# Kernel tuning notes

Measured on AMD Instinct MI355X. Metric: run time of the kernel, lower is better.

Reference implementation:

```python
import jax, jax.numpy as jnp
import numpy as np

B, T, S = 1, 8, 1024
HID, H = 1152, 16
D = HID // H  # 72
EPS = 1e-6


def rmsnorm(t, gamma):
    # t: [b,t,s,h,d], gamma: [h,d] per-head learnable scale (QKNorm)
    var = jnp.mean(jnp.square(t), axis=-1, keepdims=True)
    return t * jax.lax.rsqrt(var + EPS) * gamma


def setup_inputs() -> dict:
    key = jax.random.key(0)
    ks = jax.random.split(key, 8)
    sc = lambda fan_in: 1.0 / np.sqrt(fan_in)
    x = jax.random.normal(ks[0], (B, T, S, HID), dtype=jnp.float32)
    Wq = jax.random.normal(ks[1], (HID, HID), dtype=jnp.float32) * sc(HID)
    bq = jnp.zeros((HID,), dtype=jnp.float32)
    Wkv = jax.random.normal(ks[2], (HID, 2 * HID), dtype=jnp.float32) * sc(HID)
    bkv = jnp.zeros((2 * HID,), dtype=jnp.float32)
    q_gamma = jnp.ones((H, D), dtype=jnp.float32)
    k_gamma = jnp.ones((H, D), dtype=jnp.float32)
    Wo = jax.random.normal(ks[3], (HID, HID), dtype=jnp.float32) * sc(HID)
    return {"x": x, "Wq": Wq, "bq": bq, "Wkv": Wkv, "bkv": bkv,
            "q_gamma": q_gamma, "k_gamma": k_gamma, "Wo": Wo}


def reference(x, Wq, bq, Wkv, bkv, q_gamma, k_gamma, Wo):
    b, t, s, _ = x.shape
    q = (x @ Wq + bq).reshape(b, t, s, H, D)
    kv = x @ Wkv + bkv
    k, v = jnp.split(kv, 2, axis=-1)
    k = k.reshape(b, t, s, H, D)
    v = v.reshape(b, t, s, H, D)
    q = rmsnorm(q, q_gamma)
    k = rmsnorm(k, k_gamma)
    # NOTE: original applies no 1/sqrt(d) scaling (QKNorm replaces it)
    attn_weight = jnp.einsum('btqhd,btkhd->bthqk', q, k)
    attn = jax.nn.softmax(attn_weight, axis=-1)
    out = jnp.einsum('bthqk,btkhd->btqhd', attn, v).reshape(b, t, s, HID)
    return out @ Wo
```

## Files before the change

### kernel.cpp

```cpp
#include <hip/hip_runtime.h>


typedef __attribute__((ext_vector_type(4))) short s16x4;
typedef __attribute__((ext_vector_type(8))) short s16x8;
typedef __attribute__((ext_vector_type(4))) float f32x4;
typedef __attribute__((ext_vector_type(16))) float f32x16;

__device__ __forceinline__ unsigned short f2b(float x) {
  unsigned u = __float_as_uint(x);
  u += 0x7FFFu + ((u >> 16) & 1u);
  return (unsigned short)(u >> 16);
}
__device__ __forceinline__ float b2f(unsigned short u) {
  return __uint_as_float(((unsigned)u) << 16);
}
__device__ __forceinline__ void gld16(const void* g, void* l) {
  __builtin_amdgcn_global_load_lds(
      (const __attribute__((address_space(1))) void*)g,
      (__attribute__((address_space(3))) void*)l, 16, 0, 0);
}

__global__ __launch_bounds__(256) void cvt_bf16_kernel(const float* __restrict__ in,
                                                       unsigned short* __restrict__ out,
                                                       int n16) {
  int i = blockIdx.x * 256 + threadIdx.x;
  if (i >= n16) return;
  const float4* p = (const float4*)(in + (size_t)i * 16);
  float4 a = p[0], b = p[1], c = p[2], d = p[3];
  s16x8 r0, r1;
  r0[0] = (short)f2b(a.x); r0[1] = (short)f2b(a.y); r0[2] = (short)f2b(a.z); r0[3] = (short)f2b(a.w);
  r0[4] = (short)f2b(c.x); r0[5] = (short)f2b(c.y); r0[6] = (short)f2b(c.z); r0[7] = (short)f2b(c.w);
  r1[0] = (short)f2b(b.x); r1[1] = (short)f2b(b.y); r1[2] = (short)f2b(b.z); r1[3] = (short)f2b(b.w);
  r1[4] = (short)f2b(d.x); r1[5] = (short)f2b(d.y); r1[6] = (short)f2b(d.z); r1[7] = (short)f2b(d.w);
  *(s16x8*)(out + (size_t)i * 16) = r0;
  *(s16x8*)(out + (size_t)i * 16 + 8) = r1;
}

__global__ __launch_bounds__(256) void transpose_cvt_kernel(const float* __restrict__ W,
                                                            unsigned short* __restrict__ WT,
                                                            int K, int N) {
  __shared__ float tile[32][33];
  int n0 = blockIdx.x * 32, k0 = blockIdx.y * 32;
  int tx = threadIdx.x, ty = threadIdx.y;
#pragma unroll
  for (int i = 0; i < 4; i++)
    tile[ty + i * 8][tx] = W[(size_t)(k0 + ty + i * 8) * N + n0 + tx];
  __syncthreads();
  int stx = (tx & 19) | ((tx & 4) << 1) | ((tx & 8) >> 1);
#pragma unroll
  for (int i = 0; i < 4; i++)
    WT[(size_t)(n0 + ty + i * 8) * K + k0 + stx] = f2b(tile[tx][ty + i * 8]);
}

__global__ __launch_bounds__(256) void gemm_qkv_kernel(const unsigned short* __restrict__ A,
                                                       const unsigned short* __restrict__ BT,
                                                       const float* __restrict__ biasq,
                                                       const float* __restrict__ biaskv,
                                                       unsigned short* __restrict__ qn,
                                                       unsigned short* __restrict__ kn,
                                                       unsigned short* __restrict__ vt) {
  constexpr int K = 1152;
  constexpr int NT = K / 32;
  __shared__ __align__(16) unsigned short As[3 * 8192];
  __shared__ __align__(16) unsigned short Bs[3 * 4096];
  int tid = threadIdx.x;
  int lane = tid & 63, wave = tid >> 6;
  int wr = (wave >> 1) * 128, wc = (wave & 1) * 64;
  int l31 = lane & 31, lh = lane >> 5;
  int bid = blockIdx.x;
  int xcd = bid & 7;
  int w = bid >> 3;
  int st = w / 12, inner = w - st * 12;
  int ibx = inner % 3, iby = inner / 3;
  int bx = st * 3 + ibx;
  int by = xcd * 4 + iby;
  int brow = by * 256, bcol = bx * 128;
  const unsigned short* AsrcP[4];
  const unsigned short* BsrcP[2];
  int dstA[4], dstB[2];
#pragma unroll
  for (int i = 0; i < 4; i++) {
    int c = tid + 256 * i;
    int row = c >> 2, j = c & 3;
    AsrcP[i] = A + (size_t)(brow + row) * K + (j ^ ((row >> 1) & 3)) * 8;
    dstA[i] = (wave * 64 + 256 * i) * 8;
  }
#pragma unroll
  for (int i = 0; i < 2; i++) {
    int c = tid + 256 * i;
    int row = c >> 2, j = c & 3;
    BsrcP[i] = BT + (size_t)(bcol + row) * K + (j ^ ((row >> 1) & 3)) * 8;
    dstB[i] = (wave * 64 + 256 * i) * 8;
  }
#define STAGE(KT, BUF)                                           \
  {                                                              \
    int kb = (KT) * 32;                                          \
    gld16(AsrcP[0] + kb, &As[(BUF) * 8192 + dstA[0]]);           \
    gld16(AsrcP[1] + kb, &As[(BUF) * 8192 + dstA[1]]);           \
    gld16(AsrcP[2] + kb, &As[(BUF) * 8192 + dstA[2]]);           \
    gld16(AsrcP[3] + kb, &As[(BUF) * 8192 + dstA[3]]);           \
    gld16(BsrcP[0] + kb, &Bs[(BUF) * 4096 + dstB[0]]);           \
    gld16(BsrcP[1] + kb, &Bs[(BUF) * 4096 + dstB[1]]);           \
  }
  int fr = (l31 >> 1) & 3;
  int slotk[2] = {(lh ^ fr) * 8, ((2 + lh) ^ fr) * 8};
  STAGE(0, 0);
  STAGE(1, 1);
  f32x16 acc[4][2] = {};
  int cur = 0;
  for (int kt = 0; kt < NT; kt++) {
    if (kt < NT - 1)
      asm volatile("s_waitcnt vmcnt(6)\n\ts_barrier" ::: "memory");
    else
      asm volatile("s_waitcnt vmcnt(0)\n\ts_barrier" ::: "memory");
    if (kt + 2 < NT) {
      int nb = (cur == 0) ? 2 : cur - 1;
      STAGE(kt + 2, nb);
    }
    int ab = cur * 8192, bb = cur * 4096;
#pragma unroll
    for (int kk = 0; kk < 2; kk++) {
      int so = slotk[kk];
      s16x8 af[4], bf[2];
#pragma unroll
      for (int m = 0; m < 4; m++)
        af[m] = *(const s16x8*)&As[ab + (wr + m * 32 + l31) * 32 + so];
#pragma unroll
      for (int n = 0; n < 2; n++)
        bf[n] = *(const s16x8*)&Bs[bb + (wc + n * 32 + l31) * 32 + so];
      __builtin_amdgcn_s_setprio(1);
#pragma unroll
      for (int m = 0; m < 4; m++)
#pragma unroll
        for (int n = 0; n < 2; n++)
          acc[m][n] = __builtin_amdgcn_mfma_f32_32x32x16_bf16(af[m], bf[n], acc[m][n], 0, 0, 0);
      __builtin_amdgcn_s_setprio(0);
    }
    cur = (cur == 2) ? 0 : cur + 1;
  }
#undef STAGE
#pragma unroll
  for (int m = 0; m < 4; m++) {
#pragma unroll
    for (int n = 0; n < 2; n++) {
#pragma unroll
      for (int reg = 0; reg < 16; reg++) {
        int grow = brow + wr + m * 32 + (reg & 3) + 8 * (reg >> 2) + 4 * lh;
        int gcol = bcol + wc + n * 32 + l31;
        float v = acc[m][n][reg];
        v += (gcol < 1152) ? biasq[gcol] : biaskv[gcol - 1152];
        int t = grow >> 10, s = grow & 1023;
        if (gcol < 2304) {
          int c = (gcol < 1152) ? gcol : gcol - 1152;
          int h = c / 72, d = c - h * 72;
          unsigned short* dst = (gcol < 1152) ? qn : kn;
          dst[((size_t)((t * 16 + h) * 1024 + s)) * 96 + d] = f2b(v);
        } else {
          int c = gcol - 2304;
          int h = c / 72, d = c - h * 72;
          vt[((size_t)((t * 16 + h) * 80 + d)) * 1024 + s] = f2b(v);
        }
      }
    }
  }
}

__global__ __launch_bounds__(256) void gemm_out_kernel(const unsigned short* __restrict__ A,
                                                       const unsigned short* __restrict__ BT,
                                                       int N, int gx,
                                                       float* __restrict__ outF) {
  constexpr int K = 1152;
  constexpr int NT = K / 32;
  __shared__ __align__(16) unsigned short As[3 * 4096];
  __shared__ __align__(16) unsigned short Bs[3 * 4096];
  int tid = threadIdx.x;
  int lane = tid & 63, wave = tid >> 6;
  int wr = (wave >> 1) * 64, wc = (wave & 1) * 64;
  int l31 = lane & 31, lh = lane >> 5;
  int bid = blockIdx.x;
  int xcd = bid & 7;
  int w = bid >> 3;
  int st = w / 24, inner = w - st * 24;
  int ibx = inner % 3, iby = inner / 3;
  int bx = st * 3 + ibx;
  int by = xcd * 8 + iby;
  int brow = by * 128, bcol = bx * 128;
  const unsigned short* AsrcP[2];
  const unsigned short* BsrcP[2];
  int dst0[2];
#pragma unroll
  for (int i = 0; i < 2; i++) {
    int c = tid + 256 * i;
    int row = c >> 2, j = c & 3;
    int ch = j ^ ((row >> 1) & 3);
    AsrcP[i] = A + (size_t)(brow + row) * K + ch * 8;
    BsrcP[i] = BT + (size_t)(bcol + row) * K + ch * 8;
    dst0[i] = (wave * 64 + 256 * i) * 8;
  }
#define STAGE(KT, BUF)                                          \
  {                                                             \
    int kb = (KT) * 32;                                         \
    gld16(AsrcP[0] + kb, &As[(BUF) * 4096 + dst0[0]]);          \
    gld16(BsrcP[0] + kb, &Bs[(BUF) * 4096 + dst0[0]]);          \
    gld16(AsrcP[1] + kb, &As[(BUF) * 4096 + dst0[1]]);          \
    gld16(BsrcP[1] + kb, &Bs[(BUF) * 4096 + dst0[1]]);          \
  }
  int fr = (l31 >> 1) & 3;
  int slotk[2] = {(lh ^ fr) * 8, ((2 + lh) ^ fr) * 8};
  STAGE(0, 0);
  STAGE(1, 1);
  f32x16 acc[2][2] = {};
  int cur = 0;
  for (int kt = 0; kt < NT; kt++) {
    if (kt < NT - 1)
      asm volatile("s_waitcnt vmcnt(4)\n\ts_barrier" ::: "memory");
    else
      asm volatile("s_waitcnt vmcnt(0)\n\ts_barrier" ::: "memory");
    if (kt + 2 < NT) {
      int nb = (cur == 0) ? 2 : cur - 1;
      STAGE(kt + 2, nb);
    }
    int ab = cur * 4096;
#pragma unroll
    for (int kk = 0; kk < 2; kk++) {
      int so = slotk[kk];
      s16x8 af[2], bf[2];
#pragma unroll
      for (int m = 0; m < 2; m++)
        af[m] = *(const s16x8*)&As[ab + (wr + m * 32 + l31) * 32 + so];
#pragma unroll
      for (int n = 0; n < 2; n++)
        bf[n] = *(const s16x8*)&Bs[ab + (wc + n * 32 + l31) * 32 + so];
      __builtin_amdgcn_s_setprio(1);
#pragma unroll
      for (int m = 0; m < 2; m++)
#pragma unroll
        for (int n = 0; n < 2; n++)
          acc[m][n] = __builtin_amdgcn_mfma_f32_32x32x16_bf16(af[m], bf[n], acc[m][n], 0, 0, 0);
      __builtin_amdgcn_s_setprio(0);
    }
    cur = (cur == 2) ? 0 : cur + 1;
  }
#undef STAGE
#pragma unroll
  for (int m = 0; m < 2; m++) {
#pragma unroll
    for (int n = 0; n < 2; n++) {
#pragma unroll
      for (int reg = 0; reg < 16; reg++) {
        int grow = brow + wr + m * 32 + (reg & 3) + 8 * (reg >> 2) + 4 * lh;
        int gcol = bcol + wc + n * 32 + l31;
        outF[(size_t)grow * N + gcol] = acc[m][n][reg];
      }
    }
  }
}

__global__ __launch_bounds__(256) void rmsnorm2_kernel(unsigned short* __restrict__ qn,
                                                       unsigned short* __restrict__ kn,
                                                       const float* __restrict__ qg,
                                                       const float* __restrict__ kg) {
  int r = blockIdx.x * 4 + (threadIdx.x >> 6);
  int isK = r >= 131072;
  int g = isK ? r - 131072 : r;
  unsigned short* buf = isK ? kn : qn;
  const float* gamma = isK ? kg : qg;
  int h = (g >> 10) & 15;
  size_t base = (size_t)g * 96;
  int l = threadIdx.x & 63;
  float e0 = b2f(buf[base + l]);
  float e1 = 0.f;
  if (l < 8) e1 = b2f(buf[base + 64 + l]);
  float ss = e0 * e0 + e1 * e1;
#pragma unroll
  for (int m = 1; m < 64; m <<= 1) ss += __shfl_xor(ss, m);
  float sc = rsqrtf(ss * (1.0f / 72.0f) + 1e-6f);
  buf[base + l] = f2b(e0 * sc * gamma[h * 72 + l]);
  if (l < 32) {
    float v = 0.f;
    if (l < 8) v = e1 * sc * gamma[h * 72 + 64 + l];
    buf[base + 64 + l] = f2b(v);
  }
}

__global__ __launch_bounds__(256) void attn_kernel(const unsigned short* __restrict__ Qn,
                                                   const unsigned short* __restrict__ Kn,
                                                   const unsigned short* __restrict__ VtG,
                                                   unsigned short* __restrict__ att) {
  __shared__ unsigned short Kl[2][64][100];
  __shared__ unsigned short Vt[2][80][76];
  int tid = threadIdx.x;
  int lane = tid & 63, wave = tid >> 6;
  int l15 = lane & 15, lq = lane >> 4, kf = lq * 4;
  int bid = blockIdx.x;
  int orig = (bid & 7) * 256 + (bid >> 3);
  int qb = orig & 15, th = orig >> 4;
  int t = th >> 4, h = th & 15;
  const unsigned short* Q = Qn + (size_t)th * 1024 * 96;
  const unsigned short* Kp = Kn + (size_t)th * 1024 * 96;
  const unsigned short* Vg = VtG + (size_t)th * 80 * 1024;
  int qrow0 = qb * 64 + wave * 16;
  int krow[3], kco[3], vd[3], vco[3];
#pragma unroll
  for (int i = 0; i < 3; i++) {
    int c = tid + i * 256;
    krow[i] = c / 12;
    kco[i] = c - 12 * krow[i];
    int cc = tid + i * 256;
    vd[i] = cc >> 3;
    vco[i] = cc & 7;
  }
  bool v2 = tid < 128;
  s16x8 sk[3], sv[3];
  s16x8 qf[3];
#pragma unroll
  for (int c = 0; c < 3; c++) {
    const unsigned short* p = Q + (size_t)(qrow0 + l15) * 96 + c * 32 + kf;
    s16x4 lo = *(const s16x4*)p;
    s16x4 hi = *(const s16x4*)(p + 16);
    qf[c] = __builtin_shufflevector(lo, hi, 0, 1, 2, 3, 4, 5, 6, 7);
  }
  f32x4 o[5] = {};
  float m_r = -3.0e38f, l_r = 0.f;

#pragma unroll
  for (int i = 0; i < 3; i++)
    sk[i] = *(const s16x8*)(Kp + (size_t)krow[i] * 96 + kco[i] * 8);
#pragma unroll
  for (int i = 0; i < 2; i++)
    sv[i] = *(const s16x8*)(Vg + (size_t)vd[i] * 1024 + vco[i] * 8);
  if (v2) sv[2] = *(const s16x8*)(Vg + (size_t)vd[2] * 1024 + vco[2] * 8);
#pragma unroll
  for (int i = 0; i < 3; i++) *(s16x8*)&Kl[0][krow[i]][kco[i] * 8] = sk[i];
#pragma unroll
  for (int i = 0; i < 2; i++) *(s16x8*)&Vt[0][vd[i]][vco[i] * 8] = sv[i];
  if (v2) *(s16x8*)&Vt[0][vd[2]][vco[2] * 8] = sv[2];

  for (int tt = 0; tt < 16; tt++) {
    __syncthreads();
    int cur = tt & 1;
    if (tt < 15) {
      int kv1 = (tt + 1) * 64;
#pragma unroll
      for (int i = 0; i < 3; i++)
        sk[i] = *(const s16x8*)(Kp + (size_t)(kv1 + krow[i]) * 96 + kco[i] * 8);
#pragma unroll
      for (int i = 0; i < 2; i++)
        sv[i] = *(const s16x8*)(Vg + (size_t)vd[i] * 1024 + kv1 + vco[i] * 8);
      if (v2) sv[2] = *(const s16x8*)(Vg + (size_t)vd[2] * 1024 + kv1 + vco[2] * 8);
    }
    f32x4 st[4];
    __builtin_amdgcn_s_setprio(1);
#pragma unroll
    for (int n = 0; n < 4; n++) {
      f32x4 a = {};
#pragma unroll
      for (int c = 0; c < 3; c++) {
        s16x4 lo = *(const s16x4*)&Kl[cur][n * 16 + l15][c * 32 + kf];
        s16x4 hi = *(const s16x4*)&Kl[cur][n * 16 + l15][c * 32 + kf + 16];
        s16x8 kfr = __builtin_shufflevector(lo, hi, 0, 1, 2, 3, 4, 5, 6, 7);
        a = __builtin_amdgcn_mfma_f32_16x16x32_bf16(kfr, qf[c], a, 0, 0, 0);
      }
      st[n] = a;
    }
    __builtin_amdgcn_s_setprio(0);
    float tmax = st[0][0];
#pragma unroll
    for (int n = 0; n < 4; n++)
#pragma unroll
      for (int r = 0; r < 4; r++) tmax = fmaxf(tmax, st[n][r]);
    tmax = fmaxf(tmax, __shfl_xor(tmax, 16));
    tmax = fmaxf(tmax, __shfl_xor(tmax, 32));
    float mn = fmaxf(m_r, tmax);
    float scale = __expf(m_r - mn);
    m_r = mn;
    float sum = 0.f;
#pragma unroll
    for (int n = 0; n < 4; n++)
#pragma unroll
      for (int r = 0; r < 4; r++) {
        float p = __expf(st[n][r] - mn);
        st[n][r] = p;
        sum += p;
      }
    sum += __shfl_xor(sum, 16);
    sum += __shfl_xor(sum, 32);
    l_r = l_r * scale + sum;
#pragma unroll
    for (int r = 0; r < 4; r++) {
      float scq = __shfl(scale, 4 * lq + r);
#pragma unroll
      for (int v = 0; v < 5; v++) o[v][r] *= scq;
    }
    __builtin_amdgcn_s_setprio(1);
#pragma unroll
    for (int b = 0; b < 2; b++) {
      s16x8 pf;
#pragma unroll
      for (int j = 0; j < 8; j++) pf[j] = (short)f2b(st[2 * b + (j >> 2)][j & 3]);
#pragma unroll
      for (int v = 0; v < 5; v++) {
        s16x4 vlo = *(const s16x4*)&Vt[cur][v * 16 + l15][b * 32 + kf];
        s16x4 vhi = *(const s16x4*)&Vt[cur][v * 16 + l15][b * 32 + kf + 16];
        s16x8 vf = __builtin_shufflevector(vlo, vhi, 0, 1, 2, 3, 4, 5, 6, 7);
        o[v] = __builtin_amdgcn_mfma_f32_16x16x32_bf16(pf, vf, o[v], 0, 0, 0);
      }
    }
    __builtin_amdgcn_s_setprio(0);
    if (tt < 15) {
      int nxt = cur ^ 1;
#pragma unroll
      for (int i = 0; i < 3; i++) *(s16x8*)&Kl[nxt][krow[i]][kco[i] * 8] = sk[i];
#pragma unroll
      for (int i = 0; i < 2; i++) *(s16x8*)&Vt[nxt][vd[i]][vco[i] * 8] = sv[i];
      if (v2) *(s16x8*)&Vt[nxt][vd[2]][vco[2] * 8] = sv[2];
    }
  }
#pragma unroll
  for (int r = 0; r < 4; r++) {
    float inv = 1.0f / __shfl(l_r, 4 * lq + r);
    int qrow = qrow0 + 4 * lq + r;
    size_t rowbase = (size_t)(t * 1024 + qrow) * 1152;
#pragma unroll
    for (int v = 0; v < 5; v++) {
      int d = v * 16 + l15;
      if (d < 72) {
        int col = h * 72 + d;
        int scol = (col & ~12) | ((col & 4) << 1) | ((col & 8) >> 1);
        att[rowbase + scol] = f2b(o[v][r] * inv);
      }
    }
  }
}

extern "C" void kernel_launch(void* const* d_in, const int* in_sizes, int n_in,
                              void* d_out, int out_size, void* d_ws, size_t ws_size,
                              hipStream_t stream) {
  const float* x   = (const float*)d_in[0];
  const float* Wq  = (const float*)d_in[1];
  const float* bq  = (const float*)d_in[2];
  const float* Wkv = (const float*)d_in[3];
  const float* bkv = (const float*)d_in[4];
  const float* qg  = (const float*)d_in[5];
  const float* kg  = (const float*)d_in[6];
  const float* Wo  = (const float*)d_in[7];
  float* out = (float*)d_out;

  char* w = (char*)d_ws;
  unsigned short* xb   = (unsigned short*)w; w += (size_t)8192 * 1152 * 2;
  unsigned short* WqT  = (unsigned short*)w; w += (size_t)1152 * 1152 * 2;
  unsigned short* WkvT = (unsigned short*)w; w += (size_t)2304 * 1152 * 2;
  unsigned short* WoT  = (unsigned short*)w; w += (size_t)1152 * 1152 * 2;
  unsigned short* qn   = (unsigned short*)w; w += (size_t)128 * 1024 * 96 * 2;
  unsigned short* kn   = (unsigned short*)w; w += (size_t)128 * 1024 * 96 * 2;
  unsigned short* vt   = (unsigned short*)w; w += (size_t)128 * 80 * 1024 * 2;
  unsigned short* att  = (unsigned short*)w; w += (size_t)8192 * 1152 * 2;

  cvt_bf16_kernel<<<2304, 256, 0, stream>>>(x, xb, 9437184 / 16);
  transpose_cvt_kernel<<<dim3(36, 36), dim3(32, 8), 0, stream>>>(Wq, WqT, 1152, 1152);
  transpose_cvt_kernel<<<dim3(72, 36), dim3(32, 8), 0, stream>>>(Wkv, WkvT, 1152, 2304);
  transpose_cvt_kernel<<<dim3(36, 36), dim3(32, 8), 0, stream>>>(Wo, WoT, 1152, 1152);

  gemm_qkv_kernel<<<864, 256, 0, stream>>>(xb, WqT, bq, bkv, qn, kn, vt);
  rmsnorm2_kernel<<<65536, 256, 0, stream>>>(qn, kn, qg, kg);

  attn_kernel<<<2048, 256, 0, stream>>>(qn, kn, vt, att);

  gemm_out_kernel<<<576, 256, 0, stream>>>(att, WoT, 1152, 9, out);
}
```

Measured before the change: 308.9 us.

## Process 32 query rows per wave in attention to reuse K/V tiles

Each wave now handles two 16-row query groups, so each block covers 128 query rows and the grid is halved to 1024 blocks. Every K/V tile staged in shared memory feeds twice as many MFMAs, which halves global K/V traffic and per-tile staging and sync overhead. The cost is higher register pressure from doubled accumulators and Q fragments, plus fewer blocks in flight for occupancy.

Result: no change. 308.8 us (-0.0%).

```diff
diff --git a/kernel.cpp b/kernel.cpp
--- a/kernel.cpp
+++ b/kernel.cpp
@@ -293,13 +293,13 @@
   int lane = tid & 63, wave = tid >> 6;
   int l15 = lane & 15, lq = lane >> 4, kf = lq * 4;
   int bid = blockIdx.x;
-  int orig = (bid & 7) * 256 + (bid >> 3);
-  int qb = orig & 15, th = orig >> 4;
+  int orig = (bid & 7) * 128 + (bid >> 3);
+  int qb = orig & 7, th = orig >> 3;
   int t = th >> 4, h = th & 15;
   const unsigned short* Q = Qn + (size_t)th * 1024 * 96;
   const unsigned short* Kp = Kn + (size_t)th * 1024 * 96;
   const unsigned short* Vg = VtG + (size_t)th * 80 * 1024;
-  int qrow0 = qb * 64 + wave * 16;
+  int qrow0 = qb * 128 + wave * 32;
   int krow[3], kco[3], vd[3], vco[3];
 #pragma unroll
   for (int i = 0; i < 3; i++) {
@@ -312,16 +312,18 @@
   }
   bool v2 = tid < 128;
   s16x8 sk[3], sv[3];
-  s16x8 qf[3];
-#pragma unroll
-  for (int c = 0; c < 3; c++) {
-    const unsigned short* p = Q + (size_t)(qrow0 + l15) * 96 + c * 32 + kf;
-    s16x4 lo = *(const s16x4*)p;
-    s16x4 hi = *(const s16x4*)(p + 16);
-    qf[c] = __builtin_shufflevector(lo, hi, 0, 1, 2, 3, 4, 5, 6, 7);
-  }
-  f32x4 o[5] = {};
-  float m_r = -3.0e38f, l_r = 0.f;
+  s16x8 qf[2][3];
+#pragma unroll
+  for (int g = 0; g < 2; g++)
+#pragma unroll
+    for (int c = 0; c < 3; c++) {
+      const unsigned short* p = Q + (size_t)(qrow0 + g * 16 + l15) * 96 + c * 32 + kf;
+      s16x4 lo = *(const s16x4*)p;
+      s16x4 hi = *(const s16x4*)(p + 16);
+      qf[g][c] = __builtin_shufflevector(lo, hi, 0, 1, 2, 3, 4, 5, 6, 7);
+    }
+  f32x4 o[2][5] = {};
+  float m_r[2] = {-3.0e38f, -3.0e38f}, l_r[2] = {0.f, 0.f};
 
 #pragma unroll
   for (int i = 0; i < 3; i++)
@@ -349,64 +351,67 @@
         sv[i] = *(const s16x8*)(Vg + (size_t)vd[i] * 1024 + kv1 + vco[i] * 8);
       if (v2) sv[2] = *(const s16x8*)(Vg + (size_t)vd[2] * 1024 + kv1 + vco[2] * 8);
     }
-    f32x4 st[4];
-    __builtin_amdgcn_s_setprio(1);
-#pragma unroll
-    for (int n = 0; n < 4; n++) {
-      f32x4 a = {};
-#pragma unroll
-      for (int c = 0; c < 3; c++) {
-        s16x4 lo = *(const s16x4*)&Kl[cur][n * 16 + l15][c * 32 + kf];
-        s16x4 hi = *(const s16x4*)&Kl[cur][n * 16 + l15][c * 32 + kf + 16];
-        s16x8 kfr = __builtin_shufflevector(lo, hi, 0, 1, 2, 3, 4, 5, 6, 7);
-        a = __builtin_amdgcn_mfma_f32_16x16x32_bf16(kfr, qf[c], a, 0, 0, 0);
-      }
-      st[n] = a;
-    }
-    __builtin_amdgcn_s_setprio(0);
-    float tmax = st[0][0];
-#pragma unroll
-    for (int n = 0; n < 4; n++)
-#pragma unroll
-      for (int r = 0; r < 4; r++) tmax = fmaxf(tmax, st[n][r]);
-    tmax = fmaxf(tmax, __shfl_xor(tmax, 16));
-    tmax = fmaxf(tmax, __shfl_xor(tmax, 32));
-    float mn = fmaxf(m_r, tmax);
-    float scale = __expf(m_r - mn);
-    m_r = mn;
-    float sum = 0.f;
-#pragma unroll
-    for (int n = 0; n < 4; n++)
+#pragma unroll
+    for (int g = 0; g < 2; g++) {
+      f32x4 st[4];
+      __builtin_amdgcn_s_setprio(1);
+#pragma unroll
+      for (int n = 0; n < 4; n++) {
+        f32x4 a = {};
+#pragma unroll
+        for (int c = 0; c < 3; c++) {
+          s16x4 lo = *(const s16x4*)&Kl[cur][n * 16 + l15][c * 32 + kf];
+          s16x4 hi = *(const s16x4*)&Kl[cur][n * 16 + l15][c * 32 + kf + 16];
+          s16x8 kfr = __builtin_shufflevector(lo, hi, 0, 1, 2, 3, 4, 5, 6, 7);
+          a = __builtin_amdgcn_mfma_f32_16x16x32_bf16(kfr, qf[g][c], a, 0, 0, 0);
+        }
+        st[n] = a;
+      }
+      __builtin_amdgcn_s_setprio(0);
+      float tmax = st[0][0];
+#pragma unroll
+      for (int n = 0; n < 4; n++)
+#pragma unroll
+        for (int r = 0; r < 4; r++) tmax = fmaxf(tmax, st[n][r]);
+      tmax = fmaxf(tmax, __shfl_xor(tmax, 16));
+      tmax = fmaxf(tmax, __shfl_xor(tmax, 32));
+      float mn = fmaxf(m_r[g], tmax);
+      float scale = __expf(m_r[g] - mn);
+      m_r[g] = mn;
+      float sum = 0.f;
+#pragma unroll
+      for (int n = 0; n < 4; n++)
+#pragma unroll
+        for (int r = 0; r < 4; r++) {
+          float p = __expf(st[n][r] - mn);
+          st[n][r] = p;
+          sum += p;
+        }
+      sum += __shfl_xor(sum, 16);
+      sum += __shfl_xor(sum, 32);
+      l_r[g] = l_r[g] * scale + sum;
 #pragma unroll
       for (int r = 0; r < 4; r++) {
-        float p = __expf(st[n][r] - mn);
-        st[n][r] = p;
-        sum += p;
-      }
-    sum += __shfl_xor(sum, 16);
-    sum += __shfl_xor(sum, 32);
-    l_r = l_r * scale + sum;
-#pragma unroll
-    for (int r = 0; r < 4; r++) {
-      float scq = __shfl(scale, 4 * lq + r);
-#pragma unroll
-      for (int v = 0; v < 5; v++) o[v][r] *= scq;
-    }
-    __builtin_amdgcn_s_setprio(1);
-#pragma unroll
-    for (int b = 0; b < 2; b++) {
-      s16x8 pf;
-#pragma unroll
-      for (int j = 0; j < 8; j++) pf[j] = (short)f2b(st[2 * b + (j >> 2)][j & 3]);
-#pragma unroll
-      for (int v = 0; v < 5; v++) {
-        s16x4 vlo = *(const s16x4*)&Vt[cur][v * 16 + l15][b * 32 + kf];
-        s16x4 vhi = *(const s16x4*)&Vt[cur][v * 16 + l15][b * 32 + kf + 16];
-        s16x8 vf = __builtin_shufflevector(vlo, vhi, 0, 1, 2, 3, 4, 5, 6, 7);
-        o[v] = __builtin_amdgcn_mfma_f32_16x16x32_bf16(pf, vf, o[v], 0, 0, 0);
-      }
-    }
-    __builtin_amdgcn_s_setprio(0);
+        float scq = __shfl(scale, 4 * lq + r);
+#pragma unroll
+        for (int v = 0; v < 5; v++) o[g][v][r] *= scq;
+      }
+      __builtin_amdgcn_s_setprio(1);
+#pragma unroll
+      for (int b = 0; b < 2; b++) {
+        s16x8 pf;
+#pragma unroll
+        for (int j = 0; j < 8; j++) pf[j] = (short)f2b(st[2 * b + (j >> 2)][j & 3]);
+#pragma unroll
+        for (int v = 0; v < 5; v++) {
+          s16x4 vlo = *(const s16x4*)&Vt[cur][v * 16 + l15][b * 32 + kf];
+          s16x4 vhi = *(const s16x4*)&Vt[cur][v * 16 + l15][b * 32 + kf + 16];
+          s16x8 vf = __builtin_shufflevector(vlo, vhi, 0, 1, 2, 3, 4, 5, 6, 7);
+          o[g][v] = __builtin_amdgcn_mfma_f32_16x16x32_bf16(pf, vf, o[g][v], 0, 0, 0);
+        }
+      }
+      __builtin_amdgcn_s_setprio(0);
+    }
     if (tt < 15) {
       int nxt = cur ^ 1;
 #pragma unroll
@@ -417,20 +422,22 @@
     }
   }
 #pragma unroll
-  for (int r = 0; r < 4; r++) {
-    float inv = 1.0f / __shfl(l_r, 4 * lq + r);
-    int qrow = qrow0 + 4 * lq + r;
-    size_t rowbase = (size_t)(t * 1024 + qrow) * 1152;
-#pragma unroll
-    for (int v = 0; v < 5; v++) {
-      int d = v * 16 + l15;
-      if (d < 72) {
-        int col = h * 72 + d;
-        int scol = (col & ~12) | ((col & 4) << 1) | ((col & 8) >> 1);
-        att[rowbase + scol] = f2b(o[v][r] * inv);
-      }
-    }
-  }
+  for (int g = 0; g < 2; g++)
+#pragma unroll
+    for (int r = 0; r < 4; r++) {
+      float inv = 1.0f / __shfl(l_r[g], 4 * lq + r);
+      int qrow = qrow0 + g * 16 + 4 * lq + r;
+      size_t rowbase = (size_t)(t * 1024 + qrow) * 1152;
+#pragma unroll
+      for (int v = 0; v < 5; v++) {
+        int d = v * 16 + l15;
+        if (d < 72) {
+          int col = h * 72 + d;
+          int scol = (col & ~12) | ((col & 4) << 1) | ((col & 8) >> 1);
+          att[rowbase + scol] = f2b(o[g][v][r] * inv);
+        }
+      }
+    }
 }
 
 extern "C" void kernel_launch(void* const* d_in, const int* in_sizes, int n_in,
@@ -464,7 +471,7 @@
   gemm_qkv_kernel<<<864, 256, 0, stream>>>(xb, WqT, bq, bkv, qn, kn, vt);
   rmsnorm2_kernel<<<65536, 256, 0, stream>>>(qn, kn, qg, kg);
 
-  attn_kernel<<<2048, 256, 0, stream>>>(qn, kn, vt, att);
+  attn_kernel<<<1024, 256, 0, stream>>>(qn, kn, vt, att);
 
   gemm_out_kernel<<<576, 256, 0, stream>>>(att, WoT, 1152, 9, out);
 }
```
